# Optimization experiments

Hardware: AMD Instinct MI355X
Metric: run time of the kernel (lower is better)

Reference implementation:

```python
import jax, jax.numpy as jnp
import numpy as np

DEPTH = 2
DIM = 64
INNER = 256  # hard-coded inner_dim in Attention
HEADS = 1
N = 4096
B = 2
EPS = 1e-5


def layernorm(x, g, b):
    m = jnp.mean(x, axis=-1, keepdims=True)
    v = jnp.var(x, axis=-1, keepdims=True)
    return (x - m) * jax.lax.rsqrt(v + EPS) * g + b


def setup_inputs() -> dict:
    key = jax.random.key(0)
    ks = jax.random.split(key, 16)
    embed = jax.random.normal(ks[0], (B, N, DIM), dtype=jnp.float32)
    A = jax.random.randint(ks[1], (1, HEADS, N, N), 0, 2).astype(jnp.float32)
    s = 0.02
    return {
        "embed": embed,
        "A": A,
        "g1": jnp.ones((DEPTH, DIM), jnp.float32),
        "b1": jnp.zeros((DEPTH, DIM), jnp.float32),
        "Wqkv": jax.random.normal(ks[2], (DEPTH, DIM, INNER * 3), jnp.float32) * s,
        "Wout": jax.random.normal(ks[3], (DEPTH, INNER, DIM), jnp.float32) * s,
        "bout": jnp.zeros((DEPTH, DIM), jnp.float32),
        "g2": jnp.ones((DEPTH, DIM), jnp.float32),
        "b2": jnp.zeros((DEPTH, DIM), jnp.float32),
        "W1": jax.random.normal(ks[4], (DEPTH, DIM, DIM), jnp.float32) * s,
        "bb1": jnp.zeros((DEPTH, DIM), jnp.float32),
        "W2": jax.random.normal(ks[5], (DEPTH, DIM, DIM), jnp.float32) * s,
        "bb2": jnp.zeros((DEPTH, DIM), jnp.float32),
        "gf": jnp.ones((DIM,), jnp.float32),
        "bf": jnp.zeros((DIM,), jnp.float32),
    }


def _encoder(embed, A, g1, b1, Wqkv, Wout, bout, g2, b2, W1, bb1, W2, bb2, gf, bf):
    b, n, dim = embed.shape
    scale = dim ** (-0.5)
    dh = INNER // HEADS
    x = embed
    attn = None
    dots_softmax = None
    diag = jnp.arange(n)
    for l in range(DEPTH):
        xn = layernorm(x, g1[l], b1[l])
        qkv = xn @ Wqkv[l]  # [b, n, 3*INNER]
        q, k, v = jnp.split(qkv, 3, axis=-1)
        # [b, n, INNER] -> [b, h, n, dh]
        q = q.reshape(b, n, HEADS, dh).transpose(0, 2, 1, 3)
        k = k.reshape(b, n, HEADS, dh).transpose(0, 2, 1, 3)
        v = v.reshape(b, n, HEADS, dh).transpose(0, 2, 1, 3)
        dots = jnp.einsum("bhid,bhjd->bhij", q, k) * scale
        dots_softmax = jax.nn.softmax(dots[0, 0], axis=-1)
        # adjacency mask, then only [0][0] kept; diagonal filled with literal 1.0;
        # the original does a cpu/numpy roundtrip with .detach() -> stop_gradient.
        e = jnp.where(A > 0, dots, jnp.float32(-9e15))[0, 0]  # [n, n]
        e = e.at[diag, diag].set(1.0)
        e = jax.lax.stop_gradient(e)
        attn = jax.nn.softmax(e, axis=-1)  # [n, n], shared across b, h
        out = jnp.einsum("ij,bhjd->bhid", attn, v)  # broadcast attn over b,h
        out = out.transpose(0, 2, 1, 3).reshape(b, n, INNER)
        out = out @ Wout[l] + bout[l]
        x = xn + out  # residual onto the NORMED input (as in original)
        xm = layernorm(x, g2[l], b2[l])
        mlp = jax.nn.gelu(xm @ W1[l] + bb1[l], approximate=False) @ W2[l] + bb2[l]
        x = xm + mlp
    x = layernorm(x, gf, bf)
    return x, attn.reshape(1, 1, n, n), dots_softmax


def reference(embed, A, g1, b1, Wqkv, Wout, bout, g2, b2, W1, bb1, W2, bb2, gf, bf):
    return _encoder(embed, A, g1, b1, Wqkv, Wout, bout, g2, b2, W1, bb1, W2, bb2, gf, bf)
```

## Files before the change

### kernel.cpp

```cpp
#include <hip/hip_runtime.h>
#include <hip/hip_bf16.h>
#include <math.h>

typedef __attribute__((ext_vector_type(8))) short short8;
typedef __attribute__((ext_vector_type(4))) float f32x4;

__device__ __forceinline__ unsigned short f2bf(float x) {
    __hip_bfloat16 b = __float2bfloat16(x);
    return *reinterpret_cast<unsigned short*>(&b);
}
__device__ __forceinline__ float bf2f(unsigned short u) {
    unsigned int t = ((unsigned int)u) << 16;
    float f;
    __builtin_memcpy(&f, &t, 4);
    return f;
}
__device__ __forceinline__ float gelu_exact(float x) {
    return 0.5f * x * (1.0f + erff(x * 0.70710678118654752f));
}

__global__ __launch_bounds__(256) void k_zero(float* __restrict__ p, long n)
{
    long i = (long)blockIdx.x * 256 + threadIdx.x;
    if (i < n) p[i] = 0.f;
}

__global__ __launch_bounds__(256) void k_layernorm(
    const float* __restrict__ x, const float* __restrict__ g,
    const float* __restrict__ b, float* __restrict__ out)
{
    int wave = threadIdx.x >> 6, lane = threadIdx.x & 63;
    long row = (long)blockIdx.x * 4 + wave;
    float v = x[row * 64 + lane];
    float s = v;
    #pragma unroll
    for (int o = 32; o; o >>= 1) s += __shfl_xor(s, o);
    float m = s * (1.0f / 64.0f);
    float d = v - m;
    float q = d * d;
    #pragma unroll
    for (int o = 32; o; o >>= 1) q += __shfl_xor(q, o);
    float rstd = rsqrtf(q * (1.0f / 64.0f) + 1e-5f);
    out[row * 64 + lane] = d * rstd * g[lane] + b[lane];
}

__global__ __launch_bounds__(256) void k_wfold(
    const float* __restrict__ Wqkv, const float* __restrict__ Wout,
    float* __restrict__ Wfold)
{
    int l = blockIdx.x >> 4;
    int idx = (blockIdx.x & 15) * 256 + threadIdx.x;
    int c = idx >> 6, d = idx & 63;
    const float* Wq = Wqkv + (long)l * 64 * 768;
    const float* Wo = Wout + (long)l * 256 * 64;
    float a = 0.f;
    for (int k = 0; k < 256; ++k)
        a += Wq[c * 768 + 512 + k] * Wo[k * 64 + d];
    Wfold[l * 4096 + idx] = a;
}

__global__ __launch_bounds__(256) void k_maskpack(
    const float* __restrict__ Aadj, unsigned long long* __restrict__ mask)
{
    int row = blockIdx.x;
    int wave = threadIdx.x >> 6, lane = threadIdx.x & 63;
    for (int w = wave; w < 64; w += 4) {
        float a = Aadj[(long)row * 4096 + w * 64 + lane];
        unsigned long long m = __ballot(a > 0.f);
        if (lane == 0) mask[(long)row * 64 + w] = m;
    }
}

__global__ __launch_bounds__(256) void k_qk(
    const float* __restrict__ xn, const float* __restrict__ W,
    unsigned short* __restrict__ q, unsigned short* __restrict__ kmat)
{
    __shared__ float As[64][65];
    __shared__ float Ws[64][65];
    int tid = threadIdx.x;
    int m0 = blockIdx.x * 64, n0 = blockIdx.y * 64;
    #pragma unroll
    for (int it = 0; it < 16; ++it) {
        int idx = tid + it * 256;
        int r = idx >> 6, c = idx & 63;
        As[r][c] = xn[(long)(m0 + r) * 64 + c];
        Ws[r][c] = W[(long)r * 768 + n0 + c];
    }
    __syncthreads();
    int tx = tid & 15, ty = tid >> 4;
    float acc[4][4] = {};
    #pragma unroll
    for (int k = 0; k < 64; ++k) {
        float a[4], w[4];
        #pragma unroll
        for (int i = 0; i < 4; ++i) a[i] = As[ty * 4 + i][k];
        #pragma unroll
        for (int j = 0; j < 4; ++j) w[j] = Ws[k][tx * 4 + j];
        #pragma unroll
        for (int i = 0; i < 4; ++i)
            #pragma unroll
            for (int j = 0; j < 4; ++j) acc[i][j] += a[i] * w[j];
    }
    #pragma unroll
    for (int i = 0; i < 4; ++i) {
        long row = m0 + ty * 4 + i;
        #pragma unroll
        for (int j = 0; j < 4; ++j) {
            int col = n0 + tx * 4 + j;
            if (col < 256) q[row * 256 + col] = f2bf(acc[i][j]);
            else           kmat[row * 256 + (col - 256)] = f2bf(acc[i][j]);
        }
    }
}

__global__ __launch_bounds__(256) void k_xnw_t(
    const float* __restrict__ xn, const float* __restrict__ Wfold,
    unsigned short* __restrict__ vWT)
{
    __shared__ float As[64][65];
    __shared__ float Ws[64][65];
    int tid = threadIdx.x;
    int n0 = blockIdx.x * 64, b = blockIdx.y;
    #pragma unroll
    for (int it = 0; it < 16; ++it) {
        int idx = tid + it * 256;
        int r = idx >> 6, c = idx & 63;
        As[r][c] = xn[((long)b * 4096 + n0 + r) * 64 + c];
        Ws[r][c] = Wfold[r * 64 + c];
    }
    __syncthreads();
    int tx = tid & 15, ty = tid >> 4;
    float acc[4][4] = {};
    #pragma unroll
    for (int k = 0; k < 64; ++k) {
        float a[4], w[4];
        #pragma unroll
        for (int i = 0; i < 4; ++i) a[i] = As[ty * 4 + i][k];
        #pragma unroll
        for (int j = 0; j < 4; ++j) w[j] = Ws[k][tx * 4 + j];
        #pragma unroll
        for (int i = 0; i < 4; ++i)
            #pragma unroll
            for (int j = 0; j < 4; ++j) acc[i][j] += a[i] * w[j];
    }
    #pragma unroll
    for (int i = 0; i < 4; ++i)
        #pragma unroll
        for (int j = 0; j < 4; ++j)
            vWT[((long)b * 64 + tx * 4 + j) * 4096 + n0 + ty * 4 + i] = f2bf(acc[i][j]);
}

__global__ __launch_bounds__(256) void k_mfma_nt(
    const unsigned short* __restrict__ A, const unsigned short* __restrict__ B,
    float* __restrict__ C, unsigned short* __restrict__ Cb,
    int N, int K, float scale)
{
    __shared__ __align__(16) unsigned short As[128 * 64];
    __shared__ __align__(16) unsigned short Bs[128 * 64];
    int tid = threadIdx.x;
    int lane = tid & 63, wave = tid >> 6;
    long m0 = (long)blockIdx.x * 128, n0 = (long)blockIdx.y * 128;
    const unsigned short* Ag = A + m0 * K;
    const unsigned short* Bg = B + n0 * K;
    int wm = (wave & 1) * 64, wn = (wave >> 1) * 64;
    int fr = lane & 15, quad = lane >> 4;

    f32x4 acc[4][4];
    #pragma unroll
    for (int i = 0; i < 4; ++i)
        #pragma unroll
        for (int j = 0; j < 4; ++j) acc[i][j] = (f32x4){0.f, 0.f, 0.f, 0.f};

    for (int k0 = 0; k0 < K; k0 += 64) {
        #pragma unroll
        for (int it = 0; it < 4; ++it) {
            int c = tid + it * 256;
            int r = c >> 3, col = (c & 7) * 8;
            *(short8*)&As[c * 8] = *(const short8*)(Ag + (long)r * K + k0 + col);
            *(short8*)&Bs[c * 8] = *(const short8*)(Bg + (long)r * K + k0 + col);
        }
        __syncthreads();
        #pragma unroll
        for (int ks = 0; ks < 2; ++ks) {
            short8 af[4], bfr[4];
            #pragma unroll
            for (int i = 0; i < 4; ++i) {
                af[i]  = *(const short8*)&As[(wm + i * 16 + fr) * 64 + ks * 32 + quad * 8];
                bfr[i] = *(const short8*)&Bs[(wn + i * 16 + fr) * 64 + ks * 32 + quad * 8];
            }
            #pragma unroll
            for (int i = 0; i < 4; ++i)
                #pragma unroll
                for (int j = 0; j < 4; ++j)
                    acc[i][j] = __builtin_amdgcn_mfma_f32_16x16x32_bf16(
                        af[i], bfr[j], acc[i][j], 0, 0, 0);
        }
        __syncthreads();
    }
    #pragma unroll
    for (int i = 0; i < 4; ++i) {
        #pragma unroll
        for (int j = 0; j < 4; ++j) {
            long col = n0 + wn + j * 16 + fr;
            long rowb = m0 + wm + i * 16 + quad * 4;
            if (Cb) {
                #pragma unroll
                for (int r = 0; r < 4; ++r)
                    Cb[(rowb + r) * N + col] = f2bf(acc[i][j][r] * scale);
            } else {
                #pragma unroll
                for (int r = 0; r < 4; ++r)
                    C[(rowb + r) * N + col] = acc[i][j][r] * scale;
            }
        }
    }
}

__global__ __launch_bounds__(256) void k_mfma_splitk(
    const float* __restrict__ A, const unsigned short* __restrict__ B,
    float* __restrict__ C)
{
    __shared__ __align__(16) unsigned short As[128 * 64];
    __shared__ __align__(16) unsigned short Bs[128 * 64];
    const int K = 4096, N = 128;
    int tid = threadIdx.x;
    int lane = tid & 63, wave = tid >> 6;
    long m0 = (long)blockIdx.x * 128;
    int k0base = blockIdx.y * 512;
    const float* Ag = A + m0 * K;
    int wm = (wave & 1) * 64, wn = (wave >> 1) * 64;
    int fr = lane & 15, quad = lane >> 4;

    f32x4 acc[4][4];
    #pragma unroll
    for (int i = 0; i < 4; ++i)
        #pragma unroll
        for (int j = 0; j < 4; ++j) acc[i][j] = (f32x4){0.f, 0.f, 0.f, 0.f};

    for (int k0 = k0base; k0 < k0base + 512; k0 += 64) {
        #pragma unroll
        for (int it = 0; it < 4; ++it) {
            int c = tid + it * 256;
            int r = c >> 3, col = (c & 7) * 8;
            float4 f0 = *(const float4*)(Ag + (long)r * K + k0 + col);
            float4 f1 = *(const float4*)(Ag + (long)r * K + k0 + col + 4);
            short8 s;
            s[0] = (short)f2bf(f0.x); s[1] = (short)f2bf(f0.y);
            s[2] = (short)f2bf(f0.z); s[3] = (short)f2bf(f0.w);
            s[4] = (short)f2bf(f1.x); s[5] = (short)f2bf(f1.y);
            s[6] = (short)f2bf(f1.z); s[7] = (short)f2bf(f1.w);
            *(short8*)&As[c * 8] = s;
            *(short8*)&Bs[c * 8] = *(const short8*)(B + (long)r * K + k0 + col);
        }
        __syncthreads();
        #pragma unroll
        for (int ks = 0; ks < 2; ++ks) {
            short8 af[4], bfr[4];
            #pragma unroll
            for (int i = 0; i < 4; ++i) {
                af[i]  = *(const short8*)&As[(wm + i * 16 + fr) * 64 + ks * 32 + quad * 8];
                bfr[i] = *(const short8*)&Bs[(wn + i * 16 + fr) * 64 + ks * 32 + quad * 8];
            }
            #pragma unroll
            for (int i = 0; i < 4; ++i)
                #pragma unroll
                for (int j = 0; j < 4; ++j)
                    acc[i][j] = __builtin_amdgcn_mfma_f32_16x16x32_bf16(
                        af[i], bfr[j], acc[i][j], 0, 0, 0);
        }
        __syncthreads();
    }
    #pragma unroll
    for (int i = 0; i < 4; ++i) {
        #pragma unroll
        for (int j = 0; j < 4; ++j) {
            long col = wn + j * 16 + fr;
            long rowb = m0 + wm + i * 16 + quad * 4;
            #pragma unroll
            for (int r = 0; r < 4; ++r)
                atomicAdd(&C[(rowb + r) * N + col], acc[i][j][r]);
        }
    }
}

__global__ __launch_bounds__(256) void k_mfma_splitk_b(
    const unsigned short* __restrict__ A, const unsigned short* __restrict__ B,
    float* __restrict__ C)
{
    __shared__ __align__(16) unsigned short As[128 * 64];
    __shared__ __align__(16) unsigned short Bs[128 * 64];
    const int K = 4096, N = 128;
    int tid = threadIdx.x;
    int lane = tid & 63, wave = tid >> 6;
    long m0 = (long)blockIdx.x * 128;
    int k0base = blockIdx.y * 512;
    const unsigned short* Ag = A + m0 * K;
    int wm = (wave & 1) * 64, wn = (wave >> 1) * 64;
    int fr = lane & 15, quad = lane >> 4;

    f32x4 acc[4][4];
    #pragma unroll
    for (int i = 0; i < 4; ++i)
        #pragma unroll
        for (int j = 0; j < 4; ++j) acc[i][j] = (f32x4){0.f, 0.f, 0.f, 0.f};

    for (int k0 = k0base; k0 < k0base + 512; k0 += 64) {
        #pragma unroll
        for (int it = 0; it < 4; ++it) {
            int c = tid + it * 256;
            int r = c >> 3, col = (c & 7) * 8;
            *(short8*)&As[c * 8] = *(const short8*)(Ag + (long)r * K + k0 + col);
            *(short8*)&Bs[c * 8] = *(const short8*)(B + (long)r * K + k0 + col);
        }
        __syncthreads();
        #pragma unroll
        for (int ks = 0; ks < 2; ++ks) {
            short8 af[4], bfr[4];
            #pragma unroll
            for (int i = 0; i < 4; ++i) {
                af[i]  = *(const short8*)&As[(wm + i * 16 + fr) * 64 + ks * 32 + quad * 8];
                bfr[i] = *(const short8*)&Bs[(wn + i * 16 + fr) * 64 + ks * 32 + quad * 8];
            }
            #pragma unroll
            for (int i = 0; i < 4; ++i)
                #pragma unroll
                for (int j = 0; j < 4; ++j)
                    acc[i][j] = __builtin_amdgcn_mfma_f32_16x16x32_bf16(
                        af[i], bfr[j], acc[i][j], 0, 0, 0);
        }
        __syncthreads();
    }
    #pragma unroll
    for (int i = 0; i < 4; ++i) {
        #pragma unroll
        for (int j = 0; j < 4; ++j) {
            long col = wn + j * 16 + fr;
            long rowb = m0 + wm + i * 16 + quad * 4;
            #pragma unroll
            for (int r = 0; r < 4; ++r)
                atomicAdd(&C[(rowb + r) * N + col], acc[i][j][r]);
        }
    }
}

__device__ __forceinline__ float block_max(float v, float* red, int lane, int wave) {
    #pragma unroll
    for (int o = 32; o; o >>= 1) v = fmaxf(v, __shfl_xor(v, o));
    if (lane == 0) red[wave] = v;
    __syncthreads();
    v = fmaxf(fmaxf(red[0], red[1]), fmaxf(red[2], red[3]));
    __syncthreads();
    return v;
}
__device__ __forceinline__ float block_sum(float v, float* red, int lane, int wave) {
    #pragma unroll
    for (int o = 32; o; o >>= 1) v += __shfl_xor(v, o);
    if (lane == 0) red[wave] = v;
    __syncthreads();
    v = red[0] + red[1] + red[2] + red[3];
    __syncthreads();
    return v;
}

__global__ __launch_bounds__(256) void k_softmax_attn(
    float* __restrict__ dots, const float* __restrict__ Aadj,
    const unsigned long long* __restrict__ mask,
    float* __restrict__ attn_out, int write_ds)
{
    __shared__ float red[4];
    __shared__ unsigned long long msk[64];
    int row = blockIdx.x, tid = threadIdx.x;
    int lane = tid & 63, wave = tid >> 6;
    float* drow = dots + (long)row * 4096;
    if (mask) {
        if (tid < 64) msk[tid] = mask[(long)row * 64 + tid];
        __syncthreads();
    }
    float d[16], mv[16];
    float mmax = -1e30f, umax = -1e30f;
    #pragma unroll
    for (int i = 0; i < 16; ++i) {
        int j = tid + i * 256;
        float dv = drow[j];
        d[i] = dv;
        bool keep = mask ? ((msk[j >> 6] >> (j & 63)) & 1ull)
                         : (Aadj[(long)row * 4096 + j] > 0.f);
        float m = keep ? dv : -1e30f;
        if (j == row) m = 1.0f;
        mv[i] = m;
        mmax = fmaxf(mmax, m);
        umax = fmaxf(umax, dv);
    }
    float M1 = block_max(mmax, red, lane, wave);
    float s1 = 0.f;
    #pragma unroll
    for (int i = 0; i < 16; ++i) { float e = expf(mv[i] - M1); mv[i] = e; s1 += e; }
    s1 = block_sum(s1, red, lane, wave);
    float inv1 = 1.0f / s1;
    #pragma unroll
    for (int i = 0; i < 16; ++i)
        attn_out[(long)row * 4096 + tid + i * 256] = mv[i] * inv1;

    if (write_ds) {
        float M2 = block_max(umax, red, lane, wave);
        float s2 = 0.f;
        #pragma unroll
        for (int i = 0; i < 16; ++i) { float e = expf(d[i] - M2); d[i] = e; s2 += e; }
        s2 = block_sum(s2, red, lane, wave);
        float inv2 = 1.0f / s2;
        #pragma unroll
        for (int i = 0; i < 16; ++i)
            drow[tid + i * 256] = d[i] * inv2;
    }
}

__global__ __launch_bounds__(256) void k_softmax_b(
    const unsigned short* __restrict__ dots, const float* __restrict__ Aadj,
    const unsigned long long* __restrict__ mask,
    unsigned short* __restrict__ attn_out)
{
    __shared__ float red[4];
    __shared__ unsigned long long msk[64];
    int row = blockIdx.x, tid = threadIdx.x;
    int lane = tid & 63, wave = tid >> 6;
    const unsigned short* drow = dots + (long)row * 4096 + tid * 16;
    if (mask) {
        if (tid < 64) msk[tid] = mask[(long)row * 64 + tid];
        __syncthreads();
    }
    short8 dv0 = *(const short8*)drow;
    short8 dv1 = *(const short8*)(drow + 8);
    unsigned long long mword = mask ? msk[tid >> 2] : 0ull;
    int bitbase = (tid & 3) * 16;
    float mv[16];
    float mmax = -1e30f;
    #pragma unroll
    for (int i = 0; i < 16; ++i) {
        unsigned short u = (unsigned short)(i < 8 ? dv0[i] : dv1[i - 8]);
        float dvf = bf2f(u);
        int j = tid * 16 + i;
        bool keep = mask ? ((mword >> (bitbase + i)) & 1ull)
                         : (Aadj[(long)row * 4096 + j] > 0.f);
        float m = keep ? dvf : -1e30f;
        if (j == row) m = 1.0f;
        mv[i] = m;
        mmax = fmaxf(mmax, m);
    }
    float M1 = block_max(mmax, red, lane, wave);
    float s1 = 0.f;
    #pragma unroll
    for (int i = 0; i < 16; ++i) { float e = expf(mv[i] - M1); mv[i] = e; s1 += e; }
    s1 = block_sum(s1, red, lane, wave);
    float inv1 = 1.0f / s1;
    short8 o0, o1;
    #pragma unroll
    for (int i = 0; i < 8; ++i) {
        o0[i] = (short)f2bf(mv[i] * inv1);
        o1[i] = (short)f2bf(mv[i + 8] * inv1);
    }
    unsigned short* orow = attn_out + (long)row * 4096 + tid * 16;
    *(short8*)orow = o0;
    *(short8*)(orow + 8) = o1;
}

__global__ __launch_bounds__(256) void k_avres_ln(
    const float* __restrict__ xn, const float* __restrict__ avcat,
    const float* __restrict__ bout, const float* __restrict__ g,
    const float* __restrict__ b, float* __restrict__ out)
{
    int wave = threadIdx.x >> 6, lane = threadIdx.x & 63;
    long row = (long)blockIdx.x * 4 + wave;
    int bb = (int)(row >> 12), n = (int)(row & 4095);
    float v = xn[row * 64 + lane] + avcat[(long)n * 128 + bb * 64 + lane] + bout[lane];
    float s = v;
    #pragma unroll
    for (int o = 32; o; o >>= 1) s += __shfl_xor(s, o);
    float m = s * (1.0f / 64.0f);
    float d = v - m;
    float q = d * d;
    #pragma unroll
    for (int o = 32; o; o >>= 1) q += __shfl_xor(q, o);
    float rstd = rsqrtf(q * (1.0f / 64.0f) + 1e-5f);
    out[row * 64 + lane] = d * rstd * g[lane] + b[lane];
}

__global__ __launch_bounds__(256) void k_mlp(
    const float* __restrict__ xm,
    const float* __restrict__ W1, const float* __restrict__ bb1,
    const float* __restrict__ W2, const float* __restrict__ bb2,
    const float* __restrict__ g, const float* __restrict__ b,
    float* __restrict__ out)
{
    __shared__ float As[64][65];
    __shared__ float W1s[64][65];
    __shared__ float W2s[64][65];
    int tid = threadIdx.x;
    int m0 = blockIdx.x * 64;
    #pragma unroll
    for (int it = 0; it < 16; ++it) {
        int idx = tid + it * 256;
        int r = idx >> 6, c = idx & 63;
        As[r][c]  = xm[(long)(m0 + r) * 64 + c];
        W1s[r][c] = W1[(long)r * 64 + c];
        W2s[r][c] = W2[(long)r * 64 + c];
    }
    __syncthreads();
    int tx = tid & 15, ty = tid >> 4;
    float acc[4][4] = {};
    #pragma unroll
    for (int k = 0; k < 64; ++k) {
        float a[4], w[4];
        #pragma unroll
        for (int i = 0; i < 4; ++i) a[i] = As[ty * 4 + i][k];
        #pragma unroll
        for (int j = 0; j < 4; ++j) w[j] = W1s[k][tx * 4 + j];
        #pragma unroll
        for (int i = 0; i < 4; ++i)
            #pragma unroll
            for (int j = 0; j < 4; ++j) acc[i][j] += a[i] * w[j];
    }
    __syncthreads();
    #pragma unroll
    for (int i = 0; i < 4; ++i)
        #pragma unroll
        for (int j = 0; j < 4; ++j)
            W1s[ty * 4 + i][tx * 4 + j] = gelu_exact(acc[i][j] + bb1[tx * 4 + j]);
    __syncthreads();
    float acc2[4][4] = {};
    #pragma unroll
    for (int k = 0; k < 64; ++k) {
        float a[4], w[4];
        #pragma unroll
        for (int i = 0; i < 4; ++i) a[i] = W1s[ty * 4 + i][k];
        #pragma unroll
        for (int j = 0; j < 4; ++j) w[j] = W2s[k][tx * 4 + j];
        #pragma unroll
        for (int i = 0; i < 4; ++i)
            #pragma unroll
            for (int j = 0; j < 4; ++j) acc2[i][j] += a[i] * w[j];
    }
    #pragma unroll
    for (int i = 0; i < 4; ++i) {
        float v[4];
        float s = 0.f;
        #pragma unroll
        for (int j = 0; j < 4; ++j) {
            v[j] = acc2[i][j] + bb2[tx * 4 + j] + As[ty * 4 + i][tx * 4 + j];
            s += v[j];
        }
        #pragma unroll
        for (int o = 1; o < 16; o <<= 1) s += __shfl_xor(s, o);
        float m = s * (1.0f / 64.0f);
        float q = 0.f;
        #pragma unroll
        for (int j = 0; j < 4; ++j) { float d = v[j] - m; q += d * d; }
        #pragma unroll
        for (int o = 1; o < 16; o <<= 1) q += __shfl_xor(q, o);
        float rstd = rsqrtf(q * (1.0f / 64.0f) + 1e-5f);
        long row = m0 + ty * 4 + i;
        #pragma unroll
        for (int j = 0; j < 4; ++j) {
            int col = tx * 4 + j;
            out[row * 64 + col] = (v[j] - m) * rstd * g[col] + b[col];
        }
    }
}

extern "C" void kernel_launch(void* const* d_in, const int* in_sizes, int n_in,
                              void* d_out, int out_size, void* d_ws, size_t ws_size,
                              hipStream_t stream)
{
    const float* embed = (const float*)d_in[0];
    const float* Aadj  = (const float*)d_in[1];
    const float* g1    = (const float*)d_in[2];
    const float* b1    = (const float*)d_in[3];
    const float* Wqkv  = (const float*)d_in[4];
    const float* Wout  = (const float*)d_in[5];
    const float* bout  = (const float*)d_in[6];
    const float* g2    = (const float*)d_in[7];
    const float* b2    = (const float*)d_in[8];
    const float* W1    = (const float*)d_in[9];
    const float* bb1   = (const float*)d_in[10];
    const float* W2    = (const float*)d_in[11];
    const float* bb2   = (const float*)d_in[12];
    const float* gf    = (const float*)d_in[13];
    const float* bff   = (const float*)d_in[14];

    float* ox    = (float*)d_out;
    float* attnb = ox + 524288;
    float* dsb   = attnb + 16777216;

    if (ws_size < (10ull << 20)) {
        k_zero<<<133120, 256, 0, stream>>>(ox, 34078720l);
        return;
    }

    char* ws = (char*)d_ws;
    float*          x     = (float*)(ws + (0l << 20));
    float*          xn    = (float*)(ws + (2l << 20));
    float*          h     = (float*)(ws + (4l << 20));
    unsigned short* q     = (unsigned short*)(ws + (6l << 20));
    unsigned short* kmat  = (unsigned short*)(ws + (7l << 20));
    unsigned short* vwt   = (unsigned short*)(ws + (8l << 20));
    float*          Wfold = (float*)(ws + (9l << 20));
    unsigned long long* mask = (ws_size >= (12ull << 20))
        ? (unsigned long long*)(ws + (10l << 20)) : nullptr;
    (void)x; (void)h;

    unsigned short* dots_b = (unsigned short*)dsb;
    unsigned short* attn_b = (unsigned short*)attnb;

    if (mask) k_maskpack<<<4096, 256, 0, stream>>>(Aadj, mask);
    k_wfold<<<32, 256, 0, stream>>>(Wqkv, Wout, Wfold);

    k_layernorm<<<2048, 256, 0, stream>>>(embed, g1, b1, xn);
    k_qk<<<dim3(64, 8), 256, 0, stream>>>(xn, Wqkv, q, kmat);
    k_xnw_t<<<dim3(64, 2), 256, 0, stream>>>(xn, Wfold, vwt);
    k_mfma_nt<<<dim3(32, 32), 256, 0, stream>>>(q, kmat, nullptr, dots_b, 4096, 256, 0.125f);
    k_softmax_b<<<4096, 256, 0, stream>>>(dots_b, Aadj, mask, attn_b);
    k_zero<<<2048, 256, 0, stream>>>(ox, 524288l);
    k_mfma_splitk_b<<<dim3(32, 8), 256, 0, stream>>>(attn_b, vwt, ox);
    k_avres_ln<<<2048, 256, 0, stream>>>(xn, ox, bout, g2, b2, xn);
    k_mlp<<<128, 256, 0, stream>>>(xn, W1, bb1, W2, bb2,
                                   g1 + 64, b1 + 64, xn);

    k_qk<<<dim3(64, 8), 256, 0, stream>>>(xn, Wqkv + 64 * 768, q, kmat);
    k_xnw_t<<<dim3(64, 2), 256, 0, stream>>>(xn, Wfold + 4096, vwt);
    k_mfma_nt<<<dim3(32, 32), 256, 0, stream>>>(q, kmat, dsb, nullptr, 4096, 256, 0.125f);
    k_softmax_attn<<<4096, 256, 0, stream>>>(dsb, Aadj, mask, attnb, 1);
    k_zero<<<2048, 256, 0, stream>>>(ox, 524288l);
    k_mfma_splitk<<<dim3(32, 8), 256, 0, stream>>>(attnb, vwt, ox);
    k_avres_ln<<<2048, 256, 0, stream>>>(xn, ox, bout + 64, g2 + 64, b2 + 64, xn);
    k_mlp<<<128, 256, 0, stream>>>(xn, W1 + 4096, bb1 + 64, W2 + 4096, bb2 + 64,
                                   gf, bff, ox);
}
```

Baseline: 472.5 us.

## Fuse layer-0 attention into split-KV flash kernel with LSE combine

```diff
diff --git a/kernel.cpp b/kernel.cpp
--- a/kernel.cpp
+++ b/kernel.cpp
@@ -4,6 +4,8 @@
 
 typedef __attribute__((ext_vector_type(8))) short short8;
 typedef __attribute__((ext_vector_type(4))) float f32x4;
+
+#define NG 16
 
 __device__ __forceinline__ unsigned short f2bf(float x) {
     __hip_bfloat16 b = __float2bfloat16(x);
@@ -150,10 +152,175 @@
             vWT[((long)b * 64 + tx * 4 + j) * 4096 + n0 + ty * 4 + i] = f2bf(acc[i][j]);
 }
 
+__global__ __launch_bounds__(256) void k_flash(
+    const unsigned short* __restrict__ q, const unsigned short* __restrict__ kmat,
+    const unsigned short* __restrict__ vwt,
+    const unsigned long long* __restrict__ mask, const float* __restrict__ Aadj,
+    unsigned short* __restrict__ part,
+    float* __restrict__ stats)
+{
+    __shared__ __align__(16) unsigned short Qs[128 * 64];
+    __shared__ __align__(16) unsigned short Ks[128 * 64];
+    __shared__ __align__(16) unsigned short Ps[128 * 128];
+    int tid = threadIdx.x;
+    int lane = tid & 63, wq = tid >> 6;
+    int fr = lane & 15, quad = lane >> 4;
+    int m0 = blockIdx.x * 128;
+    int g  = blockIdx.y;
+
+    f32x4 accO[2][8];
+    #pragma unroll
+    for (int i = 0; i < 2; ++i)
+        #pragma unroll
+        for (int j = 0; j < 8; ++j) accO[i][j] = (f32x4){0.f, 0.f, 0.f, 0.f};
+    float m_run[2] = {-1e30f, -1e30f};
+    float s_run[2] = {0.f, 0.f};
+
+    for (int jt = 0; jt < 2; ++jt) {
+        int jb = g * 256 + jt * 128;
+        f32x4 accS[8][2];
+        #pragma unroll
+        for (int i = 0; i < 8; ++i)
+            #pragma unroll
+            for (int n = 0; n < 2; ++n) accS[i][n] = (f32x4){0.f, 0.f, 0.f, 0.f};
+        for (int k0 = 0; k0 < 256; k0 += 64) {
+            #pragma unroll
+            for (int it = 0; it < 4; ++it) {
+                int idx = tid + it * 256;
+                int r = idx >> 3, c8 = (idx & 7) * 8;
+                *(short8*)&Qs[idx * 8] = *(const short8*)(q    + (long)(m0 + r) * 256 + k0 + c8);
+                *(short8*)&Ks[idx * 8] = *(const short8*)(kmat + (long)(jb + r) * 256 + k0 + c8);
+            }
+            __syncthreads();
+            #pragma unroll
+            for (int ks = 0; ks < 2; ++ks) {
+                short8 ka[8], qb[2];
+                #pragma unroll
+                for (int i = 0; i < 8; ++i)
+                    ka[i] = *(const short8*)&Ks[(i * 16 + fr) * 64 + ks * 32 + quad * 8];
+                #pragma unroll
+                for (int n = 0; n < 2; ++n)
+                    qb[n] = *(const short8*)&Qs[(wq * 32 + n * 16 + fr) * 64 + ks * 32 + quad * 8];
+                #pragma unroll
+                for (int i = 0; i < 8; ++i)
+                    #pragma unroll
+                    for (int n = 0; n < 2; ++n)
+                        accS[i][n] = __builtin_amdgcn_mfma_f32_16x16x32_bf16(
+                            ka[i], qb[n], accS[i][n], 0, 0, 0);
+            }
+            __syncthreads();
+        }
+        float al[2];
+        #pragma unroll
+        for (int n = 0; n < 2; ++n) {
+            int qrow = m0 + wq * 32 + n * 16 + fr;
+            unsigned long long mw0 = 0, mw1 = 0;
+            if (mask) {
+                mw0 = mask[(long)qrow * 64 + (jb >> 6)];
+                mw1 = mask[(long)qrow * 64 + (jb >> 6) + 1];
+            }
+            float tm = -1e30f;
+            #pragma unroll
+            for (int i = 0; i < 8; ++i) {
+                #pragma unroll
+                for (int r = 0; r < 4; ++r) {
+                    int jl = i * 16 + quad * 4 + r;
+                    float v = accS[i][n][r] * 0.125f;
+                    bool keep = mask ? (((jl < 64 ? (mw0 >> jl) : (mw1 >> (jl - 64))) & 1ull) != 0)
+                                     : (Aadj[(long)qrow * 4096 + jb + jl] > 0.f);
+                    v = keep ? v : -1e30f;
+                    if (jb + jl == qrow) v = 1.0f;
+                    accS[i][n][r] = v;
+                    tm = fmaxf(tm, v);
+                }
+            }
+            tm = fmaxf(tm, __shfl_xor(tm, 16));
+            tm = fmaxf(tm, __shfl_xor(tm, 32));
+            float mnew = fmaxf(fmaxf(m_run[n], tm), -1e20f);
+            al[n] = __expf(m_run[n] - mnew);
+            m_run[n] = mnew;
+            float ts = 0.f;
+            int qrl = wq * 32 + n * 16 + fr;
+            #pragma unroll
+            for (int i = 0; i < 8; ++i) {
+                float p0 = __expf(accS[i][n][0] - mnew);
+                float p1 = __expf(accS[i][n][1] - mnew);
+                float p2 = __expf(accS[i][n][2] - mnew);
+                float p3 = __expf(accS[i][n][3] - mnew);
+                ts += (p0 + p1) + (p2 + p3);
+                unsigned int lo = (unsigned int)f2bf(p0) | ((unsigned int)f2bf(p1) << 16);
+                unsigned int hi = (unsigned int)f2bf(p2) | ((unsigned int)f2bf(p3) << 16);
+                int u = (qrl * 128 + i * 16 + quad * 4) ^ ((fr & 7) << 3);
+                *(uint2*)&Ps[u] = make_uint2(lo, hi);
+            }
+            ts += __shfl_xor(ts, 16);
+            ts += __shfl_xor(ts, 32);
+            s_run[n] = s_run[n] * al[n] + ts;
+        }
+        #pragma unroll
+        for (int ii = 0; ii < 2; ++ii) {
+            float av[4];
+            #pragma unroll
+            for (int r = 0; r < 4; ++r) av[r] = __shfl(al[ii], quad * 4 + r);
+            #pragma unroll
+            for (int nn = 0; nn < 8; ++nn)
+                #pragma unroll
+                for (int r = 0; r < 4; ++r) accO[ii][nn][r] *= av[r];
+        }
+        #pragma unroll
+        for (int it = 0; it < 4; ++it) {
+            int idx = tid + it * 256;
+            int r = idx >> 3, c8 = (idx & 7) * 8;
+            *(short8*)&Qs[idx * 8] = *(const short8*)(vwt + (long)r * 4096 + jb + c8);
+            *(short8*)&Ks[idx * 8] = *(const short8*)(vwt + (long)r * 4096 + jb + 64 + c8);
+        }
+        __syncthreads();
+        #pragma unroll
+        for (int ks4 = 0; ks4 < 4; ++ks4) {
+            const unsigned short* buf = (ks4 < 2) ? Qs : Ks;
+            int ksl = ks4 & 1;
+            short8 pa[2], vb[8];
+            #pragma unroll
+            for (int ii = 0; ii < 2; ++ii) {
+                int u = ((wq * 32 + ii * 16 + fr) * 128 + ks4 * 32 + quad * 8) ^ ((fr & 7) << 3);
+                pa[ii] = *(const short8*)&Ps[u];
+            }
+            #pragma unroll
+            for (int nn = 0; nn < 8; ++nn)
+                vb[nn] = *(const short8*)&buf[(nn * 16 + fr) * 64 + ksl * 32 + quad * 8];
+            #pragma unroll
+            for (int ii = 0; ii < 2; ++ii)
+                #pragma unroll
+                for (int nn = 0; nn < 8; ++nn)
+                    accO[ii][nn] = __builtin_amdgcn_mfma_f32_16x16x32_bf16(
+                        pa[ii], vb[nn], accO[ii][nn], 0, 0, 0);
+        }
+        __syncthreads();
+    }
+    #pragma unroll
+    for (int ii = 0; ii < 2; ++ii) {
+        #pragma unroll
+        for (int nn = 0; nn < 8; ++nn) {
+            int ch = nn * 16 + fr;
+            long rowb = m0 + wq * 32 + ii * 16 + quad * 4;
+            #pragma unroll
+            for (int r = 0; r < 4; ++r)
+                part[((long)g * 4096 + rowb + r) * 128 + ch] = f2bf(accO[ii][nn][r]);
+        }
+    }
+    if (quad == 0) {
+        #pragma unroll
+        for (int n = 0; n < 2; ++n) {
+            int qrow = m0 + wq * 32 + n * 16 + fr;
+            stats[((long)g * 4096 + qrow) * 2]     = m_run[n];
+            stats[((long)g * 4096 + qrow) * 2 + 1] = s_run[n];
+        }
+    }
+}
+
 __global__ __launch_bounds__(256) void k_mfma_nt(
     const unsigned short* __restrict__ A, const unsigned short* __restrict__ B,
-    float* __restrict__ C, unsigned short* __restrict__ Cb,
-    int N, int K, float scale)
+    float* __restrict__ C, int N, int K, float scale)
 {
     __shared__ __align__(16) unsigned short As[128 * 64];
     __shared__ __align__(16) unsigned short Bs[128 * 64];
@@ -203,15 +370,9 @@
         for (int j = 0; j < 4; ++j) {
             long col = n0 + wn + j * 16 + fr;
             long rowb = m0 + wm + i * 16 + quad * 4;
-            if (Cb) {
-                #pragma unroll
-                for (int r = 0; r < 4; ++r)
-                    Cb[(rowb + r) * N + col] = f2bf(acc[i][j][r] * scale);
-            } else {
-                #pragma unroll
-                for (int r = 0; r < 4; ++r)
-                    C[(rowb + r) * N + col] = acc[i][j][r] * scale;
-            }
+            #pragma unroll
+            for (int r = 0; r < 4; ++r)
+                C[(rowb + r) * N + col] = acc[i][j][r] * scale;
         }
     }
 }
@@ -283,66 +444,6 @@
     }
 }
 
-__global__ __launch_bounds__(256) void k_mfma_splitk_b(
-    const unsigned short* __restrict__ A, const unsigned short* __restrict__ B,
-    float* __restrict__ C)
-{
-    __shared__ __align__(16) unsigned short As[128 * 64];
-    __shared__ __align__(16) unsigned short Bs[128 * 64];
-    const int K = 4096, N = 128;
-    int tid = threadIdx.x;
-    int lane = tid & 63, wave = tid >> 6;
-    long m0 = (long)blockIdx.x * 128;
-    int k0base = blockIdx.y * 512;
-    const unsigned short* Ag = A + m0 * K;
-    int wm = (wave & 1) * 64, wn = (wave >> 1) * 64;
-    int fr = lane & 15, quad = lane >> 4;
-
-    f32x4 acc[4][4];
-    #pragma unroll
-    for (int i = 0; i < 4; ++i)
-        #pragma unroll
-        for (int j = 0; j < 4; ++j) acc[i][j] = (f32x4){0.f, 0.f, 0.f, 0.f};
-
-    for (int k0 = k0base; k0 < k0base + 512; k0 += 64) {
-        #pragma unroll
-        for (int it = 0; it < 4; ++it) {
-            int c = tid + it * 256;
-            int r = c >> 3, col = (c & 7) * 8;
-            *(short8*)&As[c * 8] = *(const short8*)(Ag + (long)r * K + k0 + col);
-            *(short8*)&Bs[c * 8] = *(const short8*)(B + (long)r * K + k0 + col);
-        }
-        __syncthreads();
-        #pragma unroll
-        for (int ks = 0; ks < 2; ++ks) {
-            short8 af[4], bfr[4];
-            #pragma unroll
-            for (int i = 0; i < 4; ++i) {
-                af[i]  = *(const short8*)&As[(wm + i * 16 + fr) * 64 + ks * 32 + quad * 8];
-                bfr[i] = *(const short8*)&Bs[(wn + i * 16 + fr) * 64 + ks * 32 + quad * 8];
-            }
-            #pragma unroll
-            for (int i = 0; i < 4; ++i)
-                #pragma unroll
-                for (int j = 0; j < 4; ++j)
-                    acc[i][j] = __builtin_amdgcn_mfma_f32_16x16x32_bf16(
-                        af[i], bfr[j], acc[i][j], 0, 0, 0);
-        }
-        __syncthreads();
-    }
-    #pragma unroll
-    for (int i = 0; i < 4; ++i) {
-        #pragma unroll
-        for (int j = 0; j < 4; ++j) {
-            long col = wn + j * 16 + fr;
-            long rowb = m0 + wm + i * 16 + quad * 4;
-            #pragma unroll
-            for (int r = 0; r < 4; ++r)
-                atomicAdd(&C[(rowb + r) * N + col], acc[i][j][r]);
-        }
-    }
-}
-
 __device__ __forceinline__ float block_max(float v, float* red, int lane, int wave) {
     #pragma unroll
     for (int o = 32; o; o >>= 1) v = fmaxf(v, __shfl_xor(v, o));
@@ -414,55 +515,6 @@
     }
 }
 
-__global__ __launch_bounds__(256) void k_softmax_b(
-    const unsigned short* __restrict__ dots, const float* __restrict__ Aadj,
-    const unsigned long long* __restrict__ mask,
-    unsigned short* __restrict__ attn_out)
-{
-    __shared__ float red[4];
-    __shared__ unsigned long long msk[64];
-    int row = blockIdx.x, tid = threadIdx.x;
-    int lane = tid & 63, wave = tid >> 6;
-    const unsigned short* drow = dots + (long)row * 4096 + tid * 16;
-    if (mask) {
-        if (tid < 64) msk[tid] = mask[(long)row * 64 + tid];
-        __syncthreads();
-    }
-    short8 dv0 = *(const short8*)drow;
-    short8 dv1 = *(const short8*)(drow + 8);
-    unsigned long long mword = mask ? msk[tid >> 2] : 0ull;
-    int bitbase = (tid & 3) * 16;
-    float mv[16];
-    float mmax = -1e30f;
-    #pragma unroll
-    for (int i = 0; i < 16; ++i) {
-        unsigned short u = (unsigned short)(i < 8 ? dv0[i] : dv1[i - 8]);
-        float dvf = bf2f(u);
-        int j = tid * 16 + i;
-        bool keep = mask ? ((mword >> (bitbase + i)) & 1ull)
-                         : (Aadj[(long)row * 4096 + j] > 0.f);
-        float m = keep ? dvf : -1e30f;
-        if (j == row) m = 1.0f;
-        mv[i] = m;
-        mmax = fmaxf(mmax, m);
-    }
-    float M1 = block_max(mmax, red, lane, wave);
-    float s1 = 0.f;
-    #pragma unroll
-    for (int i = 0; i < 16; ++i) { float e = expf(mv[i] - M1); mv[i] = e; s1 += e; }
-    s1 = block_sum(s1, red, lane, wave);
-    float inv1 = 1.0f / s1;
-    short8 o0, o1;
-    #pragma unroll
-    for (int i = 0; i < 8; ++i) {
-        o0[i] = (short)f2bf(mv[i] * inv1);
-        o1[i] = (short)f2bf(mv[i + 8] * inv1);
-    }
-    unsigned short* orow = attn_out + (long)row * 4096 + tid * 16;
-    *(short8*)orow = o0;
-    *(short8*)(orow + 8) = o1;
-}
-
 __global__ __launch_bounds__(256) void k_avres_ln(
     const float* __restrict__ xn, const float* __restrict__ avcat,
     const float* __restrict__ bout, const float* __restrict__ g,
@@ -481,6 +533,43 @@
     #pragma unroll
     for (int o = 32; o; o >>= 1) q += __shfl_xor(q, o);
     float rstd = rsqrtf(q * (1.0f / 64.0f) + 1e-5f);
+    out[row * 64 + lane] = d * rstd * g[lane] + b[lane];
+}
+
+__global__ __launch_bounds__(256) void k_avres_ln_c(
+    const float* __restrict__ xn, const unsigned short* __restrict__ part,
+    const float* __restrict__ stats, const float* __restrict__ bout,
+    const float* __restrict__ g, const float* __restrict__ b,
+    float* __restrict__ out)
+{
+    int wave = threadIdx.x >> 6, lane = threadIdx.x & 63;
+    long row = (long)blockIdx.x * 4 + wave;
+    int bb = (int)(row >> 12), n = (int)(row & 4095);
+    float sm[NG], ss[NG];
+    float ms = -1e30f;
+    #pragma unroll
+    for (int gg = 0; gg < NG; ++gg) {
+        sm[gg] = stats[((long)gg * 4096 + n) * 2];
+        ss[gg] = stats[((long)gg * 4096 + n) * 2 + 1];
+        ms = fmaxf(ms, sm[gg]);
+    }
+    float acc = 0.f, stot = 0.f;
+    #pragma unroll
+    for (int gg = 0; gg < NG; ++gg) {
+        float w = __expf(sm[gg] - ms);
+        stot += w * ss[gg];
+        acc  += w * bf2f(part[((long)gg * 4096 + n) * 128 + bb * 64 + lane]);
+    }
+    float v = xn[row * 64 + lane] + acc / stot + bout[lane];
+    float s = v;
+    #pragma unroll
+    for (int o = 32; o; o >>= 1) s += __shfl_xor(s, o);
+    float m = s * (1.0f / 64.0f);
+    float d = v - m;
+    float qv = d * d;
+    #pragma unroll
+    for (int o = 32; o; o >>= 1) qv += __shfl_xor(qv, o);
+    float rstd = rsqrtf(qv * (1.0f / 64.0f) + 1e-5f);
     out[row * 64 + lane] = d * rstd * g[lane] + b[lane];
 }
 
@@ -596,19 +685,16 @@
     }
 
     char* ws = (char*)d_ws;
-    float*          x     = (float*)(ws + (0l << 20));
     float*          xn    = (float*)(ws + (2l << 20));
-    float*          h     = (float*)(ws + (4l << 20));
     unsigned short* q     = (unsigned short*)(ws + (6l << 20));
     unsigned short* kmat  = (unsigned short*)(ws + (7l << 20));
     unsigned short* vwt   = (unsigned short*)(ws + (8l << 20));
     float*          Wfold = (float*)(ws + (9l << 20));
     unsigned long long* mask = (ws_size >= (12ull << 20))
         ? (unsigned long long*)(ws + (10l << 20)) : nullptr;
-    (void)x; (void)h;
-
-    unsigned short* dots_b = (unsigned short*)dsb;
-    unsigned short* attn_b = (unsigned short*)attnb;
+
+    unsigned short* part   = (unsigned short*)attnb;
+    float*          fstats = attnb + 4194304;
 
     if (mask) k_maskpack<<<4096, 256, 0, stream>>>(Aadj, mask);
     k_wfold<<<32, 256, 0, stream>>>(Wqkv, Wout, Wfold);
@@ -616,17 +702,14 @@
     k_layernorm<<<2048, 256, 0, stream>>>(embed, g1, b1, xn);
     k_qk<<<dim3(64, 8), 256, 0, stream>>>(xn, Wqkv, q, kmat);
     k_xnw_t<<<dim3(64, 2), 256, 0, stream>>>(xn, Wfold, vwt);
-    k_mfma_nt<<<dim3(32, 32), 256, 0, stream>>>(q, kmat, nullptr, dots_b, 4096, 256, 0.125f);
-    k_softmax_b<<<4096, 256, 0, stream>>>(dots_b, Aadj, mask, attn_b);
-    k_zero<<<2048, 256, 0, stream>>>(ox, 524288l);
-    k_mfma_splitk_b<<<dim3(32, 8), 256, 0, stream>>>(attn_b, vwt, ox);
-    k_avres_ln<<<2048, 256, 0, stream>>>(xn, ox, bout, g2, b2, xn);
+    k_flash<<<dim3(32, NG), 256, 0, stream>>>(q, kmat, vwt, mask, Aadj, part, fstats);
+    k_avres_ln_c<<<2048, 256, 0, stream>>>(xn, part, fstats, bout, g2, b2, xn);
     k_mlp<<<128, 256, 0, stream>>>(xn, W1, bb1, W2, bb2,
                                    g1 + 64, b1 + 64, xn);
 
     k_qk<<<dim3(64, 8), 256, 0, stream>>>(xn, Wqkv + 64 * 768, q, kmat);
     k_xnw_t<<<dim3(64, 2), 256, 0, stream>>>(xn, Wfold + 4096, vwt);
-    k_mfma_nt<<<dim3(32, 32), 256, 0, stream>>>(q, kmat, dsb, nullptr, 4096, 256, 0.125f);
+    k_mfma_nt<<<dim3(32, 32), 256, 0, stream>>>(q, kmat, dsb, 4096, 256, 0.125f);
     k_softmax_attn<<<4096, 256, 0, stream>>>(dsb, Aadj, mask, attnb, 1);
     k_zero<<<2048, 256, 0, stream>>>(ox, 524288l);
     k_mfma_splitk<<<dim3(32, 8), 256, 0, stream>>>(attnb, vwt, ox);
```

New measurement: 463.9 us. No clear change (-1.8%).
